# Optimization experiments

Measured on AMD Instinct MI355X. Metric: run time of the kernel, lower is better.

Reference implementation:

```python
import jax, jax.numpy as jnp
from jax import lax
import numpy as np

B, T, I, H = 4096, 200, 32, 6  # batch, seq_len, input_size, hidden


def _lstm_layer(x_seq, W_ih, W_hh, b_ih, b_hh):
    """Single unidirectional LSTM layer, PyTorch gate order (i,f,g,o).
    x_seq: [B,T,Din]. Returns (all_h [B,T,H], h_last [B,H])."""
    Bb = x_seq.shape[0]
    Hh = W_hh.shape[1]
    # Precompute input projections for all timesteps (hoisted out of the scan).
    x_proj = jnp.einsum('bti,gi->btg', x_seq, W_ih) + b_ih + b_hh  # [B,T,4H]

    def step(carry, xp_t):
        h, c = carry
        gates = xp_t + h @ W_hh.T  # [B,4H]
        i_g, f_g, g_g, o_g = jnp.split(gates, 4, axis=-1)
        i_g = jax.nn.sigmoid(i_g)
        f_g = jax.nn.sigmoid(f_g)
        g_g = jnp.tanh(g_g)
        o_g = jax.nn.sigmoid(o_g)
        c = f_g * c + i_g * g_g
        h = o_g * jnp.tanh(c)
        return (h, c), h

    init = (jnp.zeros((Bb, Hh), x_seq.dtype), jnp.zeros((Bb, Hh), x_seq.dtype))
    (h_last, _), hs = lax.scan(step, init, jnp.swapaxes(x_proj, 0, 1))  # time-major scan
    return jnp.swapaxes(hs, 0, 1), h_last


def setup_inputs() -> dict:
    key = jax.random.key(0)
    ks = jax.random.split(key, 11)
    s = 0.2  # ~ uniform(-1/sqrt(H)) scale for H=6
    inp = {
        'x': jax.random.normal(ks[0], (B, T, I), dtype=jnp.float32),
        'W_ih0': jax.random.normal(ks[1], (4 * H, I), dtype=jnp.float32) * s,
        'W_hh0': jax.random.normal(ks[2], (4 * H, H), dtype=jnp.float32) * s,
        'b_ih0': jax.random.normal(ks[3], (4 * H,), dtype=jnp.float32) * s,
        'b_hh0': jax.random.normal(ks[4], (4 * H,), dtype=jnp.float32) * s,
        'W_ih1': jax.random.normal(ks[5], (4 * H, H), dtype=jnp.float32) * s,
        'W_hh1': jax.random.normal(ks[6], (4 * H, H), dtype=jnp.float32) * s,
        'b_ih1': jax.random.normal(ks[7], (4 * H,), dtype=jnp.float32) * s,
        'b_hh1': jax.random.normal(ks[8], (4 * H,), dtype=jnp.float32) * s,
        'W_lin': jax.random.normal(ks[9], (1, H), dtype=jnp.float32) * s,
        'b_lin': jax.random.normal(ks[10], (1,), dtype=jnp.float32) * s,
    }
    return inp


def reference(x, W_ih0, W_hh0, b_ih0, b_hh0, W_ih1, W_hh1, b_ih1, b_hh1, W_lin, b_lin):
    # Layer 0 (eval mode: inter-layer dropout disabled)
    h1_seq, _ = _lstm_layer(x, W_ih0, W_hh0, b_ih0, b_hh0)
    # Layer 1
    _, h2_last = _lstm_layer(h1_seq, W_ih1, W_hh1, b_ih1, b_hh1)
    # Linear head on last layer's final hidden state: [B,1]
    return h2_last @ W_lin.T + b_lin
```

## Files before the change

### kernel.cpp

```cpp
#include <hip/hip_runtime.h>


#define BATCH 4096
#define TLEN  200
#define ISZ   32
#define HSZ   6
#define GSZ   24
#define TCH   64
#define XPITCH 28
#define XROWS (TCH + 1)

__device__ __forceinline__ float fast_sig(float x) {
    return __builtin_amdgcn_rcpf(1.0f + __expf(-x));
}
__device__ __forceinline__ float rl(float v, int l) {
    return __int_as_float(__builtin_amdgcn_readlane(__float_as_int(v), l));
}
__device__ __forceinline__ float bperm(int byteIdx, float v) {
    return __int_as_float(__builtin_amdgcn_ds_bpermute(byteIdx, __float_as_int(v)));
}

__global__ void __launch_bounds__(64)
__attribute__((amdgpu_waves_per_eu(4, 4)))
lstm_fused(
    const float* __restrict__ x,
    const float* __restrict__ Wih0, const float* __restrict__ Whh0,
    const float* __restrict__ bih0, const float* __restrict__ bhh0,
    const float* __restrict__ Wih1, const float* __restrict__ Whh1,
    const float* __restrict__ bih1, const float* __restrict__ bhh1,
    const float* __restrict__ Wlin, const float* __restrict__ blin,
    float* __restrict__ out)
{
    __shared__ __align__(16) float xp_lds[XROWS * XPITCH];

    const int lane = threadIdx.x;
    const int b    = blockIdx.x;

    const bool loHalf = (lane < 32);
    const int  rr_    = loHalf ? lane : (lane - 32);
    const bool isL0   = loHalf && (rr_ < GSZ);
    const bool isL1   = !loHalf && (rr_ < GSZ);
    const int  r      = (rr_ < GSZ) ? rr_ : 0;

    float WA[HSZ], WB[HSZ];
    float base1 = 0.0f;
#pragma unroll
    for (int j = 0; j < HSZ; ++j) { WA[j] = 0.0f; WB[j] = 0.0f; }
    if (isL0) {
#pragma unroll
        for (int j = 0; j < HSZ; ++j) WA[j] = Whh0[r * HSZ + j];
    } else if (isL1) {
#pragma unroll
        for (int j = 0; j < HSZ; ++j) { WA[j] = Wih1[r * HSZ + j]; WB[j] = Whh1[r * HSZ + j]; }
        base1 = bih1[r] + bhh1[r];
    }
    const bool tanh_lane = (r >= 12 && r < 18);
    const float mg  = tanh_lane ? 2.0f : 1.0f;
    const float sg  = tanh_lane ? 2.0f : 1.0f;
    const float tgc = tanh_lane ? -1.0f : 0.0f;

    const int sel  = loHalf ? 0 : 32;
    const int jm   = (lane - sel) % HSZ;
    const int bi_i = (sel + jm) * 4;
    const int bi_f = (sel + jm + HSZ) * 4;
    const int bi_g = (sel + jm + 2 * HSZ) * 4;
    const int bi_o = (sel + jm + 3 * HSZ) * 4;

    float c = 0.0f, h = 0.0f;

    for (int t0 = 0; t0 < TLEN; t0 += TCH) {
        const int tcl = min(TCH, TLEN - t0);
        __syncthreads();

        {
            const int tclamp = min(t0 + lane, TLEN - 1);
            const float4* xrow = (const float4*)(x + ((size_t)b * TLEN + tclamp) * ISZ);
            float4 xr[8];
#pragma unroll
            for (int q = 0; q < 8; ++q) xr[q] = xrow[q];

#pragma unroll
            for (int grp = 0; grp < 3; ++grp) {
                float acc[8];
#pragma unroll
                for (int rr = 0; rr < 8; ++rr) {
                    const int row = grp * 8 + rr;
                    float a = bih0[row] + bhh0[row];
                    const float4* wrow = (const float4*)(Wih0 + row * ISZ);
#pragma unroll
                    for (int q = 0; q < 8; ++q) {
                        float4 w = wrow[q];
                        a += w.x * xr[q].x + w.y * xr[q].y + w.z * xr[q].z + w.w * xr[q].w;
                    }
                    acc[rr] = a;
                }
                *(float4*)&xp_lds[lane * XPITCH + 8 * grp] =
                    make_float4(acc[0], acc[1], acc[2], acc[3]);
                *(float4*)&xp_lds[lane * XPITCH + 8 * grp + 4] =
                    make_float4(acc[4], acc[5], acc[6], acc[7]);
            }
        }
        __syncthreads();

        const bool lastChunk = (t0 + TCH >= TLEN);
        const int  iters = tcl + (lastChunk ? 1 : 0);
        float xp_cur = xp_lds[r];
        for (int it = 0; it < iters; ++it) {
            const int kg = t0 + it;

            const float h10 = rl(h, 0),  h11 = rl(h, 1),  h12 = rl(h, 2);
            const float h13 = rl(h, 3),  h14 = rl(h, 4),  h15 = rl(h, 5);
            const float h20 = rl(h, 32), h21 = rl(h, 33), h22 = rl(h, 34);
            const float h23 = rl(h, 35), h24 = rl(h, 36), h25 = rl(h, 37);

            const float xp_nxt = xp_lds[(it + 1) * XPITCH + r];

            const float g0 = loHalf ? xp_cur : base1;
            float a0 = fmaf(WA[0], h10, fmaf(WA[2], h12, fmaf(WA[4], h14, g0)));
            float a1 = fmaf(WA[1], h11, fmaf(WA[3], h13, WA[5] * h15));
            float b0 = fmaf(WB[0], h20, fmaf(WB[2], h22, WB[4] * h24));
            float b1 = fmaf(WB[1], h21, fmaf(WB[3], h23, WB[5] * h25));
            const float g = (a0 + a1) + (b0 + b1);
            const float a = fmaf(sg, fast_sig(mg * g), tgc);

            const float iv = bperm(bi_i, a);
            const float fv = bperm(bi_f, a);
            const float gv = bperm(bi_g, a);
            const float ov = bperm(bi_o, a);

            const float cn = fmaf(fv, c, iv * gv);
            const float th = fmaf(2.0f, fast_sig(2.0f * cn), -1.0f);
            const float hn = ov * th;

            const bool ok = loHalf || (kg >= 1);
            c = ok ? cn : c;
            h = ok ? hn : h;

            xp_cur = xp_nxt;
        }
    }

    float s = blin[0];
#pragma unroll
    for (int j = 0; j < HSZ; ++j) s = fmaf(Wlin[j], rl(h, 32 + j), s);
    if (lane == 0) out[b] = s;
}

extern "C" void kernel_launch(void* const* d_in, const int* in_sizes, int n_in,
                              void* d_out, int out_size, void* d_ws, size_t ws_size,
                              hipStream_t stream) {
    const float* x    = (const float*)d_in[0];
    const float* Wih0 = (const float*)d_in[1];
    const float* Whh0 = (const float*)d_in[2];
    const float* bih0 = (const float*)d_in[3];
    const float* bhh0 = (const float*)d_in[4];
    const float* Wih1 = (const float*)d_in[5];
    const float* Whh1 = (const float*)d_in[6];
    const float* bih1 = (const float*)d_in[7];
    const float* bhh1 = (const float*)d_in[8];
    const float* Wlin = (const float*)d_in[9];
    const float* blin = (const float*)d_in[10];
    float* out = (float*)d_out;

    lstm_fused<<<BATCH, 64, 0, stream>>>(x, Wih0, Whh0, bih0, bhh0,
                                         Wih1, Whh1, bih1, bhh1,
                                         Wlin, blin, out);
}
```

Measured before the change: 288.7 us.

## Remap gate lanes into quads and use DPP quad_perm instead of ds_bpermute

Lanes are rearranged so that the four gates (i, f, g, o) of each hidden unit sit in one quad of lanes. This lets the per-step gate exchange use DPP quad_perm moves instead of four LDS-routed ds_bpermute ops on the serial recurrence. The first timestep is peeled so the per-step layer-1 predicate select can be removed. The kernel also drops the __syncthreads (the block is a single wave) and the waves_per_eu attribute, and splits the input-projection loads into halves to lower register pressure. Risks: the readlane indices and the final head read now depend on the new strided layout, and removing the occupancy hint may change register allocation.

```diff
diff --git a/kernel.cpp b/kernel.cpp
--- a/kernel.cpp
+++ b/kernel.cpp
@@ -16,12 +16,12 @@
 __device__ __forceinline__ float rl(float v, int l) {
     return __int_as_float(__builtin_amdgcn_readlane(__float_as_int(v), l));
 }
-__device__ __forceinline__ float bperm(int byteIdx, float v) {
-    return __int_as_float(__builtin_amdgcn_ds_bpermute(byteIdx, __float_as_int(v)));
+template <int CTRL>
+__device__ __forceinline__ float qperm(float v) {
+    return __int_as_float(__builtin_amdgcn_mov_dpp(__float_as_int(v), CTRL, 0xf, 0xf, true));
 }
 
 __global__ void __launch_bounds__(64)
-__attribute__((amdgpu_waves_per_eu(4, 4)))
 lstm_fused(
     const float* __restrict__ x,
     const float* __restrict__ Wih0, const float* __restrict__ Whh0,
@@ -37,62 +37,57 @@
     const int b    = blockIdx.x;
 
     const bool loHalf = (lane < 32);
-    const int  rr_    = loHalf ? lane : (lane - 32);
-    const bool isL0   = loHalf && (rr_ < GSZ);
-    const bool isL1   = !loHalf && (rr_ < GSZ);
-    const int  r      = (rr_ < GSZ) ? rr_ : 0;
+    const int  p  = lane & 3;
+    const int  jq = (lane & 31) >> 2;
+    const int  j  = (jq < HSZ) ? jq : 0;
+    const int  r  = 6 * p + j;
 
     float WA[HSZ], WB[HSZ];
     float base1 = 0.0f;
 #pragma unroll
-    for (int j = 0; j < HSZ; ++j) { WA[j] = 0.0f; WB[j] = 0.0f; }
-    if (isL0) {
+    for (int k = 0; k < HSZ; ++k) { WA[k] = 0.0f; WB[k] = 0.0f; }
+    if (loHalf) {
 #pragma unroll
-        for (int j = 0; j < HSZ; ++j) WA[j] = Whh0[r * HSZ + j];
-    } else if (isL1) {
+        for (int k = 0; k < HSZ; ++k) WA[k] = Whh0[r * HSZ + k];
+    } else {
 #pragma unroll
-        for (int j = 0; j < HSZ; ++j) { WA[j] = Wih1[r * HSZ + j]; WB[j] = Whh1[r * HSZ + j]; }
+        for (int k = 0; k < HSZ; ++k) { WA[k] = Wih1[r * HSZ + k]; WB[k] = Whh1[r * HSZ + k]; }
         base1 = bih1[r] + bhh1[r];
     }
-    const bool tanh_lane = (r >= 12 && r < 18);
-    const float mg  = tanh_lane ? 2.0f : 1.0f;
-    const float sg  = tanh_lane ? 2.0f : 1.0f;
-    const float tgc = tanh_lane ? -1.0f : 0.0f;
-
-    const int sel  = loHalf ? 0 : 32;
-    const int jm   = (lane - sel) % HSZ;
-    const int bi_i = (sel + jm) * 4;
-    const int bi_f = (sel + jm + HSZ) * 4;
-    const int bi_g = (sel + jm + 2 * HSZ) * 4;
-    const int bi_o = (sel + jm + 3 * HSZ) * 4;
+    const float mg  = (p == 2) ? 2.0f : 1.0f;
+    const float sg  = (p == 2) ? 2.0f : 1.0f;
+    const float tgc = (p == 2) ? -1.0f : 0.0f;
 
     float c = 0.0f, h = 0.0f;
 
     for (int t0 = 0; t0 < TLEN; t0 += TCH) {
         const int tcl = min(TCH, TLEN - t0);
-        __syncthreads();
 
         {
-            const int tclamp = min(t0 + lane, TLEN - 1);
-            const float4* xrow = (const float4*)(x + ((size_t)b * TLEN + tclamp) * ISZ);
-            float4 xr[8];
-#pragma unroll
-            for (int q = 0; q < 8; ++q) xr[q] = xrow[q];
-
+            const int tIdx = min(t0 + lane, TLEN - 1);
+            const float4* xrow = (const float4*)(x + ((size_t)b * TLEN + tIdx) * ISZ);
 #pragma unroll
             for (int grp = 0; grp < 3; ++grp) {
                 float acc[8];
 #pragma unroll
-                for (int rr = 0; rr < 8; ++rr) {
-                    const int row = grp * 8 + rr;
-                    float a = bih0[row] + bhh0[row];
-                    const float4* wrow = (const float4*)(Wih0 + row * ISZ);
+                for (int rr = 0; rr < 8; ++rr)
+                    acc[rr] = bih0[grp * 8 + rr] + bhh0[grp * 8 + rr];
 #pragma unroll
-                    for (int q = 0; q < 8; ++q) {
-                        float4 w = wrow[q];
-                        a += w.x * xr[q].x + w.y * xr[q].y + w.z * xr[q].z + w.w * xr[q].w;
+                for (int kh = 0; kh < 2; ++kh) {
+                    float4 xr[4];
+#pragma unroll
+                    for (int q = 0; q < 4; ++q) xr[q] = xrow[4 * kh + q];
+#pragma unroll
+                    for (int rr = 0; rr < 8; ++rr) {
+                        const float4* wrow =
+                            (const float4*)(Wih0 + (grp * 8 + rr) * ISZ + kh * 16);
+#pragma unroll
+                        for (int q = 0; q < 4; ++q) {
+                            float4 w = wrow[q];
+                            acc[rr] += w.x * xr[q].x + w.y * xr[q].y
+                                     + w.z * xr[q].z + w.w * xr[q].w;
+                        }
                     }
-                    acc[rr] = a;
                 }
                 *(float4*)&xp_lds[lane * XPITCH + 8 * grp] =
                     make_float4(acc[0], acc[1], acc[2], acc[3]);
@@ -100,18 +95,32 @@
                     make_float4(acc[4], acc[5], acc[6], acc[7]);
             }
         }
-        __syncthreads();
 
         const bool lastChunk = (t0 + TCH >= TLEN);
         const int  iters = tcl + (lastChunk ? 1 : 0);
         float xp_cur = xp_lds[r];
-        for (int it = 0; it < iters; ++it) {
-            const int kg = t0 + it;
+        int   it0 = 0;
 
-            const float h10 = rl(h, 0),  h11 = rl(h, 1),  h12 = rl(h, 2);
-            const float h13 = rl(h, 3),  h14 = rl(h, 4),  h15 = rl(h, 5);
-            const float h20 = rl(h, 32), h21 = rl(h, 33), h22 = rl(h, 34);
-            const float h23 = rl(h, 35), h24 = rl(h, 36), h25 = rl(h, 37);
+        if (t0 == 0) {
+            const float g  = loHalf ? xp_cur : base1;
+            const float a  = fmaf(sg, fast_sig(mg * g), tgc);
+            const float iq = qperm<0x00>(a);
+            const float gq = qperm<0xAA>(a);
+            const float oq = qperm<0xFF>(a);
+            const float cn = iq * gq;
+            const float th = fmaf(2.0f, fast_sig(2.0f * cn), -1.0f);
+            const float hn = oq * th;
+            c = loHalf ? cn : 0.0f;
+            h = loHalf ? hn : 0.0f;
+            xp_cur = xp_lds[XPITCH + r];
+            it0 = 1;
+        }
+
+        for (int it = it0; it < iters; ++it) {
+            const float h10 = rl(h, 0),  h11 = rl(h, 4),  h12 = rl(h, 8);
+            const float h13 = rl(h, 12), h14 = rl(h, 16), h15 = rl(h, 20);
+            const float h20 = rl(h, 32), h21 = rl(h, 36), h22 = rl(h, 40);
+            const float h23 = rl(h, 44), h24 = rl(h, 48), h25 = rl(h, 52);
 
             const float xp_nxt = xp_lds[(it + 1) * XPITCH + r];
 
@@ -123,18 +132,14 @@
             const float g = (a0 + a1) + (b0 + b1);
             const float a = fmaf(sg, fast_sig(mg * g), tgc);
 
-            const float iv = bperm(bi_i, a);
-            const float fv = bperm(bi_f, a);
-            const float gv = bperm(bi_g, a);
-            const float ov = bperm(bi_o, a);
+            const float iq = qperm<0x00>(a);
+            const float fq = qperm<0x55>(a);
+            const float gq = qperm<0xAA>(a);
+            const float oq = qperm<0xFF>(a);
 
-            const float cn = fmaf(fv, c, iv * gv);
-            const float th = fmaf(2.0f, fast_sig(2.0f * cn), -1.0f);
-            const float hn = ov * th;
-
-            const bool ok = loHalf || (kg >= 1);
-            c = ok ? cn : c;
-            h = ok ? hn : h;
+            c = fmaf(fq, c, iq * gq);
+            const float th = fmaf(2.0f, fast_sig(2.0f * c), -1.0f);
+            h = oq * th;
 
             xp_cur = xp_nxt;
         }
@@ -142,7 +147,7 @@
 
     float s = blin[0];
 #pragma unroll
-    for (int j = 0; j < HSZ; ++j) s = fmaf(Wlin[j], rl(h, 32 + j), s);
+    for (int k = 0; k < HSZ; ++k) s = fmaf(Wlin[k], rl(h, 32 + 4 * k), s);
     if (lane == 0) out[b] = s;
 }
 
```

Result: no change. 289.9 us (+0.4%).
